# Optimization experiments

Measured on AMD Instinct MI355X. Metric: run time of the kernel, lower is better.

The kernel has to match this reference:

```python
import jax, jax.numpy as jnp
import numpy as np

EPS = 1e-4          # var_epsilon for VDP batch norm
DROP = 0.2          # dropout rate
B, HWIN, K, C, HW1, HW2, UNITS = 16, 28, 5, 16, 24, 12, 10


def setup_inputs() -> dict:
    key = jax.random.key(0)
    k0, k1, k2, k3 = jax.random.split(key, 4)
    x = jax.random.normal(k0, (B, HWIN, HWIN, 1), dtype=jnp.float32)
    w_mu_conv = 0.05 * jax.random.normal(k1, (K, K, 1, C), dtype=jnp.float32)
    w_sigma_conv = jnp.full((C,), -6.9, dtype=jnp.float32)   # ini_sigma
    w_mu_fc = 0.05 * jax.random.normal(k2, (C * HW2 * HW2, UNITS), dtype=jnp.float32)
    w_sigma_fc = jnp.full((UNITS,), -6.9, dtype=jnp.float32)
    # keep-mask for dropout (True = kept), keep prob = 1 - DROP
    drop_mask = jax.random.bernoulli(k3, 1.0 - DROP, (B, HW2, HW2, C))
    return {"x": x, "drop_mask": drop_mask, "w_mu_conv": w_mu_conv,
            "w_sigma_conv": w_sigma_conv, "w_mu_fc": w_mu_fc,
            "w_sigma_fc": w_sigma_fc}


def reference(x, drop_mask, w_mu_conv, w_sigma_conv, w_mu_fc, w_sigma_fc):
    b = x.shape[0]
    p1 = HW1 * HW1      # 576
    p2 = HW2 * HW2      # 144

    # ---- VDP_first_Conv: conv mean + Sigma = softplus(w_sigma) * X X^T ----
    mu = jax.lax.conv_general_dilated(
        x, w_mu_conv, (1, 1), 'VALID',
        dimension_numbers=('NHWC', 'HWIO', 'NHWC'))            # [B,24,24,16]
    # patches: in_channels=1 so channel-major vs spatial-major ordering agree
    patches = jax.lax.conv_general_dilated_patches(
        x, (K, K), (1, 1), 'VALID',
        dimension_numbers=('NHWC', 'HWIO', 'NHWC'))            # [B,24,24,25]
    Xm = patches.reshape(b, p1, K * K)                          # [B,576,25]
    XXT = jnp.einsum('bip,bjp->bij', Xm, Xm)                    # [B,576,576]
    sigma = XXT[..., None] * jax.nn.softplus(w_sigma_conv)      # [B,576,576,16]

    # ---- VDPBatch_Normalization ----
    mean = mu.mean(axis=(0, 1, 2))
    var = mu.var(axis=(0, 1, 2))
    mu = (mu - mean) / jnp.sqrt(var + EPS)
    sigma = sigma / (var + EPS)

    # ---- VDPELU: Sigma *= g g^T with g = d elu / d mu ----
    g = jnp.where(mu > 0, 1.0, jnp.exp(mu))                     # elu'(x)
    mu = jax.nn.elu(mu)
    gf = g.reshape(b, p1, C)
    sigma = sigma * gf[:, :, None, :] * gf[:, None, :, :]

    # ---- VDP_MaxPooling 2x2/2 (24 divisible by 2 -> SAME == no pad) ----
    w = mu.reshape(b, HW2, 2, HW2, 2, C).transpose(0, 1, 3, 2, 4, 5)
    w = w.reshape(b, HW2, HW2, 4, C)                            # window flat (dy,dx)
    arg = jnp.argmax(w, axis=3)                                 # [B,12,12,16]
    mu = jnp.max(w, axis=3)                                     # [B,12,12,16]
    ii = jnp.arange(HW2)
    yy = 2 * ii[None, :, None, None] + arg // 2
    xx = 2 * ii[None, None, :, None] + arg % 2
    idx = yy * HW1 + xx                                         # flat index into 576
    idx_c = idx.transpose(0, 3, 1, 2).reshape(b, C, p2)         # [B,16,144]
    Sc = sigma.transpose(0, 3, 1, 2)                            # [B,16,576,576]
    Sc = jnp.take_along_axis(Sc, idx_c[:, :, :, None], axis=2)  # gather rows
    Sc = jnp.take_along_axis(Sc, idx_c[:, :, None, :], axis=3)  # gather cols -> [B,16,144,144]

    # ---- VDPDropout (training) ----
    scale = 1.0 / (1.0 - DROP)
    keep = drop_mask.astype(mu.dtype)                           # [B,12,12,16]
    mu = mu * keep * scale
    m = keep.transpose(0, 3, 1, 2).reshape(b, C, p2)
    Sc = (scale ** 2) * Sc * m[:, :, :, None] * m[:, :, None, :]

    # ---- VDP_Flatten_and_FC ----
    mu_flat = mu.reshape(b, -1)                                 # NHWC flatten
    mu_out = mu_flat @ w_mu_fc                                  # [B,10]
    W1 = w_mu_fc.reshape(C, p2, UNITS)                          # as in original code
    S1 = jnp.einsum('ciu,bcij,cjv->buv', W1, Sc, W1)            # sum_c W^T Sigma W
    sp = jax.nn.softplus(w_sigma_fc)                            # [10]
    tr = jnp.trace(Sc, axis1=2, axis2=3).sum(axis=1)            # [B]
    diag = sp[None, :] * (tr[:, None] + jnp.sum(mu_flat * mu_flat, axis=1)[:, None])
    Sigma_out = S1 + diag[:, :, None] * jnp.eye(UNITS, dtype=S1.dtype)
    return mu_out, Sigma_out
```

## Files before the change

kernel.cpp:

```cpp
#include <hip/hip_runtime.h>
#include <math.h>

#define EPSV   1e-4f
#define DSCALE 1.25f

#define XSTR 30
#define XIMG 840
#define QPAD 148
#define FLAG_MAGIC 0x1F2E3D4C


__device__ __forceinline__ float wave_sum(float v) {
#pragma unroll
    for (int off = 32; off > 0; off >>= 1) v += __shfl_down(v, off, 64);
    return v;
}

#define AG_LD(p)    __hip_atomic_load((p), __ATOMIC_RELAXED, __HIP_MEMORY_SCOPE_AGENT)
#define AG_ST(p, v) __hip_atomic_store((p), (v), __ATOMIC_RELAXED, __HIP_MEMORY_SCOPE_AGENT)

__global__ __launch_bounds__(256) void kFused(
    const float* __restrict__ x,
    const int*   __restrict__ dmask,
    const float* __restrict__ wconv,
    const float* __restrict__ wsconv,
    const float* __restrict__ wfc,
    const float* __restrict__ wsfc,
    float* __restrict__ moP, float* __restrict__ s1P, float* __restrict__ tmP,
    int* __restrict__ flagB, int* __restrict__ flagA, float* __restrict__ dataA,
    int* __restrict__ flagS, float* __restrict__ dataS,
    float* __restrict__ out)
{
    __shared__ __align__(16) float xa_s[XIMG];
    __shared__ __align__(16) float W1_s[1440];
    __shared__ __align__(8)  float W2_s[1440];
    __shared__ __align__(16) float fWT_s[10 * QPAD];
    __shared__ __align__(16) float XgT_s[25 * QPAD];
    __shared__ float w_s[25];
    __shared__ float red_s[8];
    __shared__ float f_s[144], mud_s[144];
    __shared__ int   I_s[144];
    __shared__ float T_s[250];
    __shared__ float stat_s[8];
    __shared__ float spfc_s[10];
    __shared__ float tmg_s[16];

    const int bc = blockIdx.x, b = bc & 15, c = bc >> 4, t = threadIdx.x;

    const int   dm    = (t < 144) ? dmask[b * 2304 + t * 16 + c] : 0;
    const float wsc_v = wsconv[c];

    {
        const float4* x4 = (const float4*)(x + b * 784);
        if (t < 196) {
            const int r = t / 7, c4 = (t - r * 7) * 4;
            const float4 v = x4[t];
            float* dst = &xa_s[r * XSTR + c4];
            ((float2*)dst)[0] = make_float2(v.x, v.y);
            ((float2*)dst)[1] = make_float2(v.z, v.w);
        }
    }
    {
        const float4* wfc4 = (const float4*)wfc;
        for (int j4 = t; j4 < 360; j4 += 256)
            ((float4*)W1_s)[j4] = wfc4[c * 360 + j4];
    }
    {
        const float2* wfc2 = (const float2*)wfc;
        for (int j2 = t; j2 < 720; j2 += 256) {
            const int q = j2 / 5, uh = j2 - q * 5;
            ((float2*)W2_s)[j2] = wfc2[(q * 16 + c) * 5 + uh];
        }
    }
    if (t < 25) w_s[t] = wconv[t * 16 + c];
    if (t < 10) spfc_s[t] = log1pf(expf(wsfc[t]));
    __syncthreads();

    float best = 0.f, pn = 0.f;
    float psum_part = 0.f, psq_part = 0.f;
    if (t < 144) {
        const int h = t / 12, w2 = t - h * 12;
        const int y0 = 2 * h, x0 = 2 * w2;
        float xr[6][6];
#pragma unroll
        for (int i = 0; i < 6; i++) {
            const float2* row = (const float2*)&xa_s[(y0 + i) * XSTR + x0];
#pragma unroll
            for (int k = 0; k < 3; k++) {
                const float2 v = row[k];
                xr[i][2 * k] = v.x; xr[i][2 * k + 1] = v.y;
            }
        }
        float v00 = 0.f, v01 = 0.f, v10 = 0.f, v11 = 0.f;
#pragma unroll
        for (int i = 0; i < 5; i++)
#pragma unroll
            for (int j = 0; j < 5; j++) {
                const float wv = w_s[i * 5 + j];
                v00 = fmaf(xr[i][j],         wv, v00);
                v01 = fmaf(xr[i][j + 1],     wv, v01);
                v10 = fmaf(xr[i + 1][j],     wv, v10);
                v11 = fmaf(xr[i + 1][j + 1], wv, v11);
            }
        psum_part = v00 + v01 + v10 + v11;
        psq_part  = v00 * v00 + v01 * v01 + v10 * v10 + v11 * v11;
        best = v00; int arg = 0;
        if (v01 > best) { best = v01; arg = 1; }
        if (v10 > best) { best = v10; arg = 2; }
        if (v11 > best) { best = v11; arg = 3; }
        float pn0 = 0.f, pn1 = 0.f, pn2 = 0.f, pn3 = 0.f;
#pragma unroll
        for (int i = 0; i < 5; i++)
#pragma unroll
            for (int j = 0; j < 5; j++) {
                pn0 = fmaf(xr[i][j],         xr[i][j],         pn0);
                pn1 = fmaf(xr[i][j + 1],     xr[i][j + 1],     pn1);
                pn2 = fmaf(xr[i + 1][j],     xr[i + 1][j],     pn2);
                pn3 = fmaf(xr[i + 1][j + 1], xr[i + 1][j + 1], pn3);
            }
        pn = (arg == 0) ? pn0 : (arg == 1) ? pn1 : (arg == 2) ? pn2 : pn3;
        I_s[t] = (y0 + (arg >> 1)) * XSTR + (x0 + (arg & 1));
    }
    {
        const float wsum1 = wave_sum(psum_part), wsum2 = wave_sum(psq_part);
        if ((t & 63) == 0) { red_s[t >> 6] = wsum1; red_s[4 + (t >> 6)] = wsum2; }
    }
    __syncthreads();

    if (t == 0) {
        const float ts = red_s[0] + red_s[1] + red_s[2] + red_s[3];
        const float tq = red_s[4] + red_s[5] + red_s[6] + red_s[7];
        const int ln = bc * 32;
        AG_ST(&dataA[ln], ts); AG_ST(&dataA[ln + 1], tq);
        asm volatile("s_waitcnt vmcnt(0)" ::: "memory");
        AG_ST(&flagA[ln], FLAG_MAGIC);
    }

    if (b == 0 && t < 16) {
        const int ln = (c * 16 + t) * 32;
        while (AG_LD(&flagA[ln]) != FLAG_MAGIC) __builtin_amdgcn_s_sleep(1);
        AG_ST(&flagA[ln], 0);
        float pa = AG_LD(&dataA[ln]), pb = AG_LD(&dataA[ln + 1]);
#pragma unroll
        for (int off = 8; off > 0; off >>= 1) {
            pa += __shfl_down(pa, off, 64);
            pb += __shfl_down(pb, off, 64);
        }
        pa = __shfl(pa, 0, 64); pb = __shfl(pb, 0, 64);
        const float mean = pa * (1.f / 9216.f);
        const float var  = pb * (1.f / 9216.f) - mean * mean;
        const float istd = 1.f / sqrtf(var + EPSV);
        const float scv  = log1pf(expf(wsc_v)) / (var + EPSV);
        AG_ST(&dataS[ln], mean); AG_ST(&dataS[ln + 1], istd); AG_ST(&dataS[ln + 2], scv);
        asm volatile("s_waitcnt vmcnt(0)" ::: "memory");
        AG_ST(&flagS[ln], FLAG_MAGIC);
    }

    for (int e = t; e < 3600; e += 256) {
        const int p = e / 144, q = e - p * 144;
        XgT_s[p * QPAD + q] = xa_s[I_s[q] + (p / 5) * XSTR + (p % 5)];
    }

    if (t == 0) {
        const int ln = bc * 32;
        while (AG_LD(&flagS[ln]) != FLAG_MAGIC) __builtin_amdgcn_s_sleep(1);
        AG_ST(&flagS[ln], 0);
        stat_s[0] = AG_LD(&dataS[ln]);
        stat_s[1] = AG_LD(&dataS[ln + 1]);
        stat_s[2] = AG_LD(&dataS[ln + 2]);
    }
    __syncthreads();

    float trv = 0.f, mmv = 0.f;
    if (t < 144) {
        const float vn = (best - stat_s[0]) * stat_s[1];
        const float m  = (dm != 0) ? 1.f : 0.f;
        const float g  = vn > 0.f ? 1.f : expf(vn);
        const float el = vn > 0.f ? vn  : expm1f(vn);
        const float fq = DSCALE * m * g;
        const float md = DSCALE * m * el;
        f_s[t] = fq; mud_s[t] = md;
        trv = stat_s[2] * fq * fq * pn;
        mmv = md * md;
    }
    {
        const float wt = wave_sum(trv), wm = wave_sum(mmv);
        if ((t & 63) == 0) { red_s[t >> 6] = wt; red_s[4 + (t >> 6)] = wm; }
    }
    __syncthreads();

    for (int j = t; j < 1440; j += 256) {
        const int q = j / 10, u = j - q * 10;
        fWT_s[u * QPAD + q] = f_s[q] * W1_s[j];
    }
    if (t == 0)
        stat_s[3] = red_s[0] + red_s[1] + red_s[2] + red_s[3]
                  + red_s[4] + red_s[5] + red_s[6] + red_s[7];
    __syncthreads();

    if (t < 250) {
        const int p = t / 10, u = t - (t / 10) * 10;
        const float4* fa = (const float4*)&fWT_s[u * QPAD];
        const float4* xg = (const float4*)&XgT_s[p * QPAD];
        float acc = 0.f;
#pragma unroll 6
        for (int k = 0; k < 36; k++) {
            const float4 a = fa[k], g4 = xg[k];
            acc = fmaf(a.x, g4.x, acc);
            acc = fmaf(a.y, g4.y, acc);
            acc = fmaf(a.z, g4.z, acc);
            acc = fmaf(a.w, g4.w, acc);
        }
        T_s[t] = acc;
    }
    __syncthreads();

    float sig_val = 0.f, mu_val = 0.f;
    if (t < 100) {
        const int u = t / 10, v = t - (t / 10) * 10;
        float acc = 0.f;
#pragma unroll
        for (int p = 0; p < 25; p++)
            acc = fmaf(T_s[p * 10 + u], T_s[p * 10 + v], acc);
        sig_val = stat_s[2] * acc;
    } else if (t < 110) {
        const int u = t - 100;
        float acc = 0.f;
#pragma unroll 8
        for (int q = 0; q < 144; q++)
            acc = fmaf(mud_s[q], W2_s[q * 10 + u], acc);
        mu_val = acc;
    }

    if (c != 0) {
        if (t < 100)       AG_ST(&s1P[bc * 100 + t], sig_val);
        else if (t < 110)  AG_ST(&moP[bc * 10 + (t - 100)], mu_val);
        else if (t == 110) AG_ST(&tmP[bc], stat_s[3]);
        asm volatile("s_waitcnt vmcnt(0)" ::: "memory");
        __syncthreads();
        if (t == 0) AG_ST(&flagB[bc * 32], FLAG_MAGIC);
    } else {
        if (t < 15) {
            const int idx = ((t + 1) * 16 + b) * 32;
            while (AG_LD(&flagB[idx]) != FLAG_MAGIC) __builtin_amdgcn_s_sleep(2);
            AG_ST(&flagB[idx], 0);
        }
        __syncthreads();
        if (t < 15) tmg_s[t] = AG_LD(&tmP[(t + 1) * 16 + b]);
        __syncthreads();
        if (t == 0) {
            float a = stat_s[3];
            for (int i = 0; i < 15; i++) a += tmg_s[i];
            stat_s[5] = a;
        }
        __syncthreads();
        if (t < 100) {
            const int u = t / 10, v = t - (t / 10) * 10;
            float acc = sig_val;
#pragma unroll
            for (int cc = 1; cc < 16; cc++)
                acc += AG_LD(&s1P[(cc * 16 + b) * 100 + t]);
            if (u == v) acc += spfc_s[u] * stat_s[5];
            out[160 + b * 100 + t] = acc;
        } else if (t < 110) {
            const int u = t - 100;
            float acc = mu_val;
#pragma unroll
            for (int cc = 1; cc < 16; cc++)
                acc += AG_LD(&moP[(cc * 16 + b) * 10 + u]);
            out[b * 10 + u] = acc;
        }
    }
}

extern "C" void kernel_launch(void* const* d_in, const int* in_sizes, int n_in,
                              void* d_out, int out_size, void* d_ws, size_t ws_size,
                              hipStream_t stream) {
    const float* x      = (const float*)d_in[0];
    const int*   dmask  = (const int*)d_in[1];
    const float* wconv  = (const float*)d_in[2];
    const float* wsconv = (const float*)d_in[3];
    const float* wfc    = (const float*)d_in[4];
    const float* wsfc   = (const float*)d_in[5];
    float* out = (float*)d_out;

    float* ws    = (float*)d_ws;
    float* moP   = ws;
    float* s1P   = ws + 2560;
    float* tmP   = ws + 28160;
    int*   flagB = (int*)(ws + 28416);
    int*   flagA = (int*)(ws + 36608);
    float* dataA = ws + 44800;
    int*   flagS = (int*)(ws + 52992);
    float* dataS = ws + 61184;

    kFused<<<256, 256, 0, stream>>>(x, dmask, wconv, wsconv, wfc, wsfc,
                                    moP, s1P, tmP, flagB, flagA, dataA,
                                    flagS, dataS, out);
}
```

Before: 18.34 us.

## Replace two-hop batch-norm stat barrier with all-to-all flag exchange per channel

Previously each block published its partial sums, one leader block per channel gathered all 16 partials, computed mean/var, and published them through a second flag round. Now every block signals all 16 peers in its channel directly and each block reduces the 16 partials itself. This removes one cross-block round trip and the serial dependence on the leader block, in exchange for redundant stat computation and 16x more flag stores and polls.

```diff
diff --git a/kernel.cpp b/kernel.cpp
--- a/kernel.cpp
+++ b/kernel.cpp
@@ -28,7 +28,6 @@
     const float* __restrict__ wsfc,
     float* __restrict__ moP, float* __restrict__ s1P, float* __restrict__ tmP,
     int* __restrict__ flagB, int* __restrict__ flagA, float* __restrict__ dataA,
-    int* __restrict__ flagS, float* __restrict__ dataS,
     float* __restrict__ out)
 {
     __shared__ __align__(16) float xa_s[XIMG];
@@ -132,42 +131,37 @@
         const float tq = red_s[4] + red_s[5] + red_s[6] + red_s[7];
         const int ln = bc * 32;
         AG_ST(&dataA[ln], ts); AG_ST(&dataA[ln + 1], tq);
-        asm volatile("s_waitcnt vmcnt(0)" ::: "memory");
-        AG_ST(&flagA[ln], FLAG_MAGIC);
-    }
-
-    if (b == 0 && t < 16) {
-        const int ln = (c * 16 + t) * 32;
-        while (AG_LD(&flagA[ln]) != FLAG_MAGIC) __builtin_amdgcn_s_sleep(1);
-        AG_ST(&flagA[ln], 0);
-        float pa = AG_LD(&dataA[ln]), pb = AG_LD(&dataA[ln + 1]);
-#pragma unroll
-        for (int off = 8; off > 0; off >>= 1) {
-            pa += __shfl_down(pa, off, 64);
-            pb += __shfl_down(pb, off, 64);
-        }
-        pa = __shfl(pa, 0, 64); pb = __shfl(pb, 0, 64);
-        const float mean = pa * (1.f / 9216.f);
-        const float var  = pb * (1.f / 9216.f) - mean * mean;
-        const float istd = 1.f / sqrtf(var + EPSV);
-        const float scv  = log1pf(expf(wsc_v)) / (var + EPSV);
-        AG_ST(&dataS[ln], mean); AG_ST(&dataS[ln + 1], istd); AG_ST(&dataS[ln + 2], scv);
-        asm volatile("s_waitcnt vmcnt(0)" ::: "memory");
-        AG_ST(&flagS[ln], FLAG_MAGIC);
-    }
+    }
+    asm volatile("s_waitcnt vmcnt(0)" ::: "memory");
+    if (t < 16)
+        AG_ST(&flagA[(c * 16 + t) * 32 + b], FLAG_MAGIC);
 
     for (int e = t; e < 3600; e += 256) {
         const int p = e / 144, q = e - p * 144;
         XgT_s[p * QPAD + q] = xa_s[I_s[q] + (p / 5) * XSTR + (p % 5)];
     }
 
-    if (t == 0) {
-        const int ln = bc * 32;
-        while (AG_LD(&flagS[ln]) != FLAG_MAGIC) __builtin_amdgcn_s_sleep(1);
-        AG_ST(&flagS[ln], 0);
-        stat_s[0] = AG_LD(&dataS[ln]);
-        stat_s[1] = AG_LD(&dataS[ln + 1]);
-        stat_s[2] = AG_LD(&dataS[ln + 2]);
+    if (t < 16) {
+        int* fl = &flagA[(c * 16 + b) * 32 + t];
+        while (AG_LD(fl) != FLAG_MAGIC) __builtin_amdgcn_s_sleep(1);
+        AG_ST(fl, 0);
+    }
+    asm volatile("s_waitcnt vmcnt(0)" ::: "memory");
+    if (t < 16) {
+        float pa = AG_LD(&dataA[(c * 16 + t) * 32]);
+        float pb = AG_LD(&dataA[(c * 16 + t) * 32 + 1]);
+#pragma unroll
+        for (int off = 8; off > 0; off >>= 1) {
+            pa += __shfl_xor(pa, off, 64);
+            pb += __shfl_xor(pb, off, 64);
+        }
+        if (t == 0) {
+            const float mean = pa * (1.f / 9216.f);
+            const float var  = pb * (1.f / 9216.f) - mean * mean;
+            stat_s[0] = mean;
+            stat_s[1] = 1.f / sqrtf(var + EPSV);
+            stat_s[2] = log1pf(expf(wsc_v)) / (var + EPSV);
+        }
     }
     __syncthreads();
 
@@ -245,6 +239,7 @@
             while (AG_LD(&flagB[idx]) != FLAG_MAGIC) __builtin_amdgcn_s_sleep(2);
             AG_ST(&flagB[idx], 0);
         }
+        asm volatile("s_waitcnt vmcnt(0)" ::: "memory");
         __syncthreads();
         if (t < 15) tmg_s[t] = AG_LD(&tmP[(t + 1) * 16 + b]);
         __syncthreads();
@@ -291,10 +286,7 @@
     int*   flagB = (int*)(ws + 28416);
     int*   flagA = (int*)(ws + 36608);
     float* dataA = ws + 44800;
-    int*   flagS = (int*)(ws + 52992);
-    float* dataS = ws + 61184;
 
     kFused<<<256, 256, 0, stream>>>(x, dmask, wconv, wsconv, wfc, wsfc,
-                                    moP, s1P, tmP, flagB, flagA, dataA,
-                                    flagS, dataS, out);
+                                    moP, s1P, tmP, flagB, flagA, dataA, out);
 }
```

After: 18.03 us. About the same (-1.6%).
